# Kernel tuning notes

Hardware: AMD Instinct MI355X
Metric: run time of the kernel (lower is better)

The kernel has to match this reference:

```python
import jax, jax.numpy as jnp
import numpy as np

B, T, H, D = 2, 4096, 16, 64
CHUNK = 64          # chunk_size / prefill_chunk_size
P = 2               # polynomial degree (only deg=2 supported)
SCALE = 0.125       # 1/sqrt(head_dim)
E = D * (D + 1) // 2  # expanded (symmetric) feature dim = 2080

_I, _J = np.triu_indices(D)
_COEF = np.where(_I == _J, 1.0, np.sqrt(2.0)).astype(np.float32)

def _phi(x):
    """Degree-2 symmetric feature map: phi(a).phi(b) == (a.b)**2. [..., D] -> [..., E]."""
    return x[..., _I] * x[..., _J] * jnp.asarray(_COEF, dtype=x.dtype)

def setup_inputs() -> dict:
    rng = jax.random.key(0)
    k0, k1, k2, k3, k4, k5 = jax.random.split(rng, 6)
    query = jax.random.normal(k0, (B, T, H, D), dtype=jnp.float32)
    key = jax.random.normal(k1, (B, T, H, D), dtype=jnp.float32)
    value = jax.random.normal(k2, (B, T, H, D), dtype=jnp.float32)
    # gate holds per-token log decay (log_G): small negative values
    gate = -0.05 * jax.random.uniform(k3, (B, T, H), dtype=jnp.float32)
    initial_state = 0.01 * jax.random.normal(k4, (B, H, E, D), dtype=jnp.float32)
    initial_sk = 0.01 * jax.random.normal(k5, (B, H, E), dtype=jnp.float32)
    return {"query": query, "key": key, "value": value, "gate": gate,
            "initial_state": initial_state, "initial_sk": initial_sk}

def _power_retention(query, key, value, gate, initial_state, initial_sk):
    C = CHUNK
    N = T // C
    # [B,T,H,*] -> chunked [B,H,N,C,*]
    q = query.transpose(0, 2, 1, 3).reshape(B, H, N, C, D)
    k = key.transpose(0, 2, 1, 3).reshape(B, H, N, C, D)
    v = value.transpose(0, 2, 1, 3).reshape(B, H, N, C, D)
    g = gate.transpose(0, 2, 1).reshape(B, H, N, C)

    cg = jnp.cumsum(g, axis=-1)     # cumulative log-gate within chunk [B,H,N,C]
    gsum = cg[..., -1]              # total chunk log-gate [B,H,N]

    # chunk axis to scan position 0
    qs = jnp.moveaxis(q, 2, 0)      # [N,B,H,C,D]
    ks = jnp.moveaxis(k, 2, 0)
    vs = jnp.moveaxis(v, 2, 0)
    cgs = jnp.moveaxis(cg, 2, 0)    # [N,B,H,C]
    gsums = jnp.moveaxis(gsum, 2, 0)  # [N,B,H]

    mask = jnp.tril(jnp.ones((C, C), dtype=bool))

    def step(carry, xs):
        S, sk = carry               # S: [B,H,E,D], sk: [B,H,E]
        qc, kc, vc, cgc, gs = xs    # [B,H,C,D], ..., [B,H,C], [B,H]
        # intra-chunk: degree-2 power attention with gating decay, causal
        qk = jnp.einsum('bhcd,bhmd->bhcm', qc, kc) * SCALE
        dec = jnp.exp(cgc[..., :, None] - cgc[..., None, :])
        s = jnp.where(mask, (qk ** P) * dec, 0.0)
        num = jnp.einsum('bhcm,bhmd->bhcd', s, vc)
        den = s.sum(-1)
        # inter-chunk: read carried state through feature map
        pq = _phi(qc) * (SCALE ** P)           # [B,H,C,E]
        qdec = jnp.exp(cgc)                    # decay from chunk start
        num = num + qdec[..., None] * jnp.einsum('bhce,bhed->bhcd', pq, S)
        den = den + qdec * jnp.einsum('bhce,bhe->bhc', pq, sk)
        # state update: decay old state by full-chunk gate, add new keys
        pk = _phi(kc) * jnp.exp(gs[..., None] - cgc)[..., None]  # [B,H,C,E]
        S = jnp.exp(gs)[..., None, None] * S + jnp.einsum('bhce,bhcd->bhed', pk, vc)
        sk = jnp.exp(gs)[..., None] * sk + pk.sum(2)
        out = num / jnp.maximum(den, 1.0)[..., None]
        return (S, sk), out

    (Sf, skf), outs = jax.lax.scan(jax.checkpoint(step), (initial_state, initial_sk),
                                   (qs, ks, vs, cgs, gsums))
    # outs: [N,B,H,C,D] -> [B,T,H,D]
    out = jnp.moveaxis(outs, 0, 2).reshape(B, H, T, D).transpose(0, 2, 1, 3)
    return out

def reference(query, key, value, gate, initial_state, initial_sk):
    return _power_retention(query, key, value, gate, initial_state, initial_sk)
```

## Files before the change

kernel.cpp:

```cpp
#include <hip/hip_runtime.h>


#define B_ 2
#define T_ 4096
#define H_ 16
#define D_ 64
#define CHUNK_ 64
#define NCH_ 64
#define E_ 2080
#define EH_ 8
#define NBLK_ 36
#define EPAD_ 288
#define NKS_ 9
#define STR_ 296
#define OUTN_ 8388608

typedef __attribute__((ext_vector_type(8))) _Float16 half8v;
typedef __attribute__((ext_vector_type(4))) float floatx4;

union U8 { half8v h; unsigned u[4]; ushort s[8]; };

static __device__ __forceinline__ float wave_iscan(float g, int lane) {
    #pragma unroll
    for (int off = 1; off < 64; off <<= 1) {
        float o = __shfl_up(g, off, 64);
        if (lane >= off) g += o;
    }
    return g;
}

typedef const __attribute__((address_space(1))) unsigned int* gas1_t;
typedef __attribute__((address_space(3))) unsigned int* las3_t;
static __device__ __forceinline__ void gload16(const void* g, void* l) {
    __builtin_amdgcn_global_load_lds((gas1_t)g, (las3_t)l, 16, 0, 0);
}

__global__ __launch_bounds__(256) void prep_kernel(
    const float* __restrict__ q, const float* __restrict__ k, const float* __restrict__ v,
    const float* __restrict__ gate,
    _Float16* __restrict__ qh, _Float16* __restrict__ kh, _Float16* __restrict__ khT,
    _Float16* __restrict__ vhT, float* __restrict__ gse_buf)
{
    const int bid = blockIdx.x;
    const int bh = bid >> 6, n = bid & 63;
    const int b = bh >> 4, h = bh & 15;
    const int t0 = n * CHUNK_;
    const int tid = threadIdx.x;

    __shared__ float cgs[64];
    __shared__ float tbuf[64 * 68];

    if (tid < 64) {
        float g = gate[((size_t)(b * T_ + t0) + tid) * H_ + h];
        cgs[tid] = wave_iscan(g, tid);
    }
    __syncthreads();
    const float gs = cgs[63];
    if (tid == 0) gse_buf[bid] = __expf(gs);

    const int c = tid >> 2, dq = (tid & 3) * 16;
    const size_t gbase = ((size_t)(b * T_ + t0 + c) * H_ + h) * 64 + dq;
    const size_t obase = (size_t)bid * 4096;

    {
        float qsc = 0.125f * __expf(0.5f * cgs[c]);
        #pragma unroll
        for (int g8 = 0; g8 < 2; ++g8) {
            float4 a0 = *(const float4*)(q + gbase + g8 * 8);
            float4 a1 = *(const float4*)(q + gbase + g8 * 8 + 4);
            half8v hv;
            hv[0] = (_Float16)(a0.x * qsc); hv[1] = (_Float16)(a0.y * qsc);
            hv[2] = (_Float16)(a0.z * qsc); hv[3] = (_Float16)(a0.w * qsc);
            hv[4] = (_Float16)(a1.x * qsc); hv[5] = (_Float16)(a1.y * qsc);
            hv[6] = (_Float16)(a1.z * qsc); hv[7] = (_Float16)(a1.w * qsc);
            int grp = (dq >> 3) + g8;
            *(half8v*)&qh[obase + (size_t)(c * 64) + ((grp ^ (c & 7)) << 3)] = hv;
        }
    }
    {
        float ksc = __expf(0.5f * (gs - cgs[c]));
        float4 sa[4];
        #pragma unroll
        for (int i = 0; i < 4; ++i) {
            float4 a = *(const float4*)(k + gbase + i * 4);
            sa[i].x = a.x * ksc; sa[i].y = a.y * ksc;
            sa[i].z = a.z * ksc; sa[i].w = a.w * ksc;
            *(float4*)&tbuf[c * 68 + dq + i * 4] = sa[i];
        }
        #pragma unroll
        for (int g8 = 0; g8 < 2; ++g8) {
            half8v hv;
            hv[0] = (_Float16)sa[g8 * 2].x;     hv[1] = (_Float16)sa[g8 * 2].y;
            hv[2] = (_Float16)sa[g8 * 2].z;     hv[3] = (_Float16)sa[g8 * 2].w;
            hv[4] = (_Float16)sa[g8 * 2 + 1].x; hv[5] = (_Float16)sa[g8 * 2 + 1].y;
            hv[6] = (_Float16)sa[g8 * 2 + 1].z; hv[7] = (_Float16)sa[g8 * 2 + 1].w;
            int grp = (dq >> 3) + g8;
            *(half8v*)&kh[obase + (size_t)(c * 64) + ((grp ^ (c & 7)) << 3)] = hv;
        }
    }
    __syncthreads();
    {
        int d = tid & 63, f = (d & 7) ^ (d >> 3);
        #pragma unroll
        for (int gg = 0; gg < 2; ++gg) {
            int cg = (tid >> 6) * 2 + gg;
            half8v hv;
            #pragma unroll
            for (int j = 0; j < 8; ++j) hv[j] = (_Float16)tbuf[(cg * 8 + j) * 68 + d];
            *(half8v*)&khT[obase + (size_t)(d * 64) + ((cg ^ f) << 3)] = hv;
        }
    }
    __syncthreads();
    {
        #pragma unroll
        for (int i = 0; i < 4; ++i)
            *(float4*)&tbuf[c * 68 + dq + i * 4] = *(const float4*)(v + gbase + i * 4);
    }
    __syncthreads();
    {
        int d = tid & 63, dl = d & 31, f = (dl & 7) ^ (dl >> 3);
        #pragma unroll
        for (int gg = 0; gg < 2; ++gg) {
            int cg = (tid >> 6) * 2 + gg;
            half8v hv;
            #pragma unroll
            for (int j = 0; j < 8; ++j) hv[j] = (_Float16)tbuf[(cg * 8 + j) * 68 + d];
            *(half8v*)&vhT[obase + (size_t)(d * 64) + ((cg ^ f) << 3)] = hv;
        }
    }
}

__global__ __launch_bounds__(512, 2) void scan_kernel(
    const _Float16* __restrict__ qh, const _Float16* __restrict__ khT,
    const _Float16* __restrict__ vhT, const float* __restrict__ gse_buf,
    const float* __restrict__ S0, const float* __restrict__ sk0,
    float* __restrict__ den_buf, _Float16* __restrict__ part)
{
    const int bid = blockIdx.x;
    const int bh = (bid & 7) * 4 + (bid >> 6);
    const int eh = (bid >> 3) & 7;
    const int tid = threadIdx.x, lane = tid & 63, w = tid >> 6;
    const int nlane = lane & 15, quad = lane >> 4;

    __shared__ __align__(16) _Float16 sT[2][64 * STR_];
    __shared__ __align__(16) _Float16 kTs[2][4096];
    __shared__ __align__(16) _Float16 qsh[2][4096];
    __shared__ __align__(16) _Float16 vTs[2][4096];
    __shared__ __align__(16) _Float16 sk_s[2][EPAD_];
    __shared__ int blk_s[NBLK_];

    for (int t = tid; t < NBLK_; t += 512) {
        int g = eh * NBLK_ + t;
        int i = 0;
        while (g >= 8 - (i >> 3)) { g -= 8 - (i >> 3); ++i; }
        int jb = (i >> 3) + g;
        blk_s[t] = i | (jb << 8);
    }
    __syncthreads();

    const _Float16* qsrc = qh + (size_t)(bh * NCH_) * 4096;
    const _Float16* ksrc = khT + (size_t)(bh * NCH_) * 4096;
    const _Float16* vsrc = vhT + (size_t)(bh * NCH_) * 4096;

    gload16(qsrc + tid * 8, &qsh[0][tid * 8]);
    gload16(ksrc + tid * 8, &kTs[0][tid * 8]);
    gload16(vsrc + tid * 8, &vTs[0][tid * 8]);

    for (int e = tid; e < EPAD_; e += 512) {
        int bv = blk_s[e >> 3];
        int i = bv & 255, j8 = (bv >> 8) * 8 + (e & 7);
        float sv = 0.f;
        if (j8 >= i) {
            int er = (i * (129 - i)) / 2 + (j8 - i);
            float coef = (j8 == i) ? 1.f : 1.41421356237f;
            sv = sk0[(size_t)bh * E_ + er] * coef;
        }
        sk_s[0][e] = (_Float16)sv;
    }
    for (int p = tid; p < 64 * EPAD_; p += 512) {
        int d = p / EPAD_;
        int e = p - d * EPAD_;
        int bv = blk_s[e >> 3];
        int i = bv & 255, j8 = (bv >> 8) * 8 + (e & 7);
        float sv = 0.f;
        if (j8 >= i) {
            int er = (i * (129 - i)) / 2 + (j8 - i);
            float coef = (j8 == i) ? 1.f : 1.41421356237f;
            sv = S0[((size_t)bh * E_ + er) * 64 + d] * coef;
        }
        int col8 = e >> 3, gsw = (d >> 2) & 3;
        int pc = ((col8 & ~3) | ((col8 & 3) ^ gsw)) * 8 + (e & 7);
        sT[0][d * STR_ + pc] = (_Float16)sv;
    }

    const int mt = w & 3, nth = w >> 2;
    const int c_row = mt * 16 + nlane;
    const bool den_w = (w < 4);
    const int NTS = (w < 2) ? 3 : 2;

    floatx4 res[3][4];
    floatx4 resk[3];
    #pragma unroll
    for (int ts = 0; ts < 3; ++ts) {
        #pragma unroll
        for (int m = 0; m < 4; ++m) res[ts][m] = (floatx4){0.f, 0.f, 0.f, 0.f};
        resk[ts] = (floatx4){0.f, 0.f, 0.f, 0.f};
        if (ts >= NTS) continue;
        int tile = w + 8 * ts;
        int e = tile * 16 + nlane;
        int bv = blk_s[e >> 3];
        int i = bv & 255, j8 = (bv >> 8) * 8 + (e & 7);
        if (j8 >= i) {
            int er = (i * (129 - i)) / 2 + (j8 - i);
            float coef = (j8 == i) ? 1.f : 1.41421356237f;
            #pragma unroll
            for (int m = 0; m < 4; ++m) {
                floatx4 t4 = *(const floatx4*)&S0[((size_t)bh * E_ + er) * 64 + m * 16 + quad * 4];
                #pragma unroll
                for (int r = 0; r < 4; ++r) res[ts][m][r] = t4[r] * coef;
            }
            if (quad == 0) resk[ts][0] = sk0[(size_t)bh * E_ + er] * coef;
        }
    }

    int qiu_off[NKS_], qrow_off[NKS_];
    #pragma unroll
    for (int ks = 0; ks < NKS_; ++ks) {
        int bv = blk_s[ks * 4 + quad];
        int ib = bv & 255, jb = bv >> 8;
        qiu_off[ks]  = (c_row * 64 + (((ib >> 3) ^ (c_row & 7)) << 3) + (ib & 7)) * 2;
        qrow_off[ks] = (c_row * 64 + ((jb ^ (c_row & 7)) << 3)) * 2;
    }
    const int swzb = (quad ^ ((nlane >> 2) & 3)) << 3;
    const int b0o0 = ((nth * 32 + nlane) * STR_ + swzb) * 2;
    const int b0o1 = ((nth * 32 + 16 + nlane) * STR_ + swzb) * 2;

    int pa_off[3], pb_off[3], stw_off[3], eidx[3];
    unsigned m2sp[3];
    #pragma unroll
    for (int ts = 0; ts < 3; ++ts) {
        pa_off[ts] = pb_off[ts] = stw_off[ts] = eidx[ts] = 0; m2sp[ts] = 0;
        if (ts >= NTS) continue;
        int tile = w + 8 * ts, e = tile * 16 + nlane;
        int bv = blk_s[e >> 3];
        int ib = bv & 255, j8 = (bv >> 8) * 8 + (e & 7);
        int fib = (ib & 7) ^ (ib >> 3), fj8 = (j8 & 7) ^ (j8 >> 3);
        pa_off[ts] = (ib * 64 + ((quad ^ fib) << 3)) * 2;
        pb_off[ts] = (j8 * 64 + ((quad ^ fj8) << 3)) * 2;
        int col8 = e >> 3;
        int pc = ((col8 & ~3) | ((col8 & 3) ^ quad)) * 8 + (e & 7);
        stw_off[ts] = (quad * 4 * STR_ + pc) * 2;
        eidx[ts] = e;
        unsigned hv = (j8 < ib) ? 0u : ((j8 == ib) ? 0x3C00u : 0x4000u);
        m2sp[ts] = (hv << 16) | hv;
    }
    int af_off[4];
    #pragma unroll
    for (int m = 0; m < 4; ++m) {
        int row = m * 16 + nlane, dl = row & 31;
        int fr = (dl & 7) ^ (dl >> 3);
        af_off[m] = (row * 64 + ((quad ^ fr) << 3)) * 2;
    }
    half8v af_sk = (half8v){0, 0, 0, 0, 0, 0, 0, 0};
    if (nlane == 0) af_sk = (half8v){1, 1, 1, 1, 1, 1, 1, 1};

    _Float16* ppart = part + (size_t)eh * OUTN_ + (((size_t)bh * T_) << 6) + nth * 32 + nlane;

    __syncthreads();

    for (int n = 0; n < NCH_; ++n) {
        const int cur = n & 1, nxt = cur ^ 1;

        if (n + 1 < NCH_) {
            gload16(qsrc + (size_t)(n + 1) * 4096 + tid * 8, &qsh[nxt][tid * 8]);
            gload16(ksrc + (size_t)(n + 1) * 4096 + tid * 8, &kTs[nxt][tid * 8]);
            gload16(vsrc + (size_t)(n + 1) * 4096 + tid * 8, &vTs[nxt][tid * 8]);
        }
        const float gsev = gse_buf[bh * NCH_ + n];

        {
            const char* qb = (const char*)&qsh[cur][0];
            const char* sb = (const char*)&sT[cur][0];
            floatx4 acc0 = {0.f, 0.f, 0.f, 0.f};
            floatx4 acc1 = {0.f, 0.f, 0.f, 0.f};
            floatx4 accd = {0.f, 0.f, 0.f, 0.f};
            #pragma unroll
            for (int ks = 0; ks < NKS_; ++ks) {
                ushort qiu = *(const ushort*)(qb + qiu_off[ks]);
                unsigned qi2 = ((unsigned)qiu << 16) | qiu;
                U8 qv; qv.u[0] = qi2; qv.u[1] = qi2; qv.u[2] = qi2; qv.u[3] = qi2;
                half8v qrow = *(const half8v*)(qb + qrow_off[ks]);
                half8v afr = qv.h * qrow;
                half8v b00 = *(const half8v*)(sb + b0o0 + ks * 64);
                half8v b01 = *(const half8v*)(sb + b0o1 + ks * 64);
                acc0 = __builtin_amdgcn_mfma_f32_16x16x32_f16(afr, b00, acc0, 0, 0, 0);
                acc1 = __builtin_amdgcn_mfma_f32_16x16x32_f16(afr, b01, acc1, 0, 0, 0);
                if (den_w) {
                    half8v b1 = (half8v){0, 0, 0, 0, 0, 0, 0, 0};
                    if (nlane == 0) b1 = *(const half8v*)&sk_s[cur][ks * 32 + quad * 8];
                    accd = __builtin_amdgcn_mfma_f32_16x16x32_f16(afr, b1, accd, 0, 0, 0);
                }
            }
            _Float16* pp = ppart + ((size_t)(n * CHUNK_ + mt * 16 + quad * 4) << 6);
            #pragma unroll
            for (int r = 0; r < 4; ++r) {
                pp[(size_t)r << 6] = (_Float16)acc0[r];
                pp[((size_t)r << 6) + 16] = (_Float16)acc1[r];
            }
            if (den_w && nlane == 0) {
                #pragma unroll
                for (int r = 0; r < 4; ++r)
                    atomicAdd(&den_buf[(size_t)bh * T_ + n * CHUNK_ + mt * 16 + quad * 4 + r], accd[r]);
            }
        }

        if (n < NCH_ - 1) {
            const char* kb = (const char*)&kTs[cur][0];
            const char* vb = (const char*)&vTs[cur][0];
            #pragma unroll
            for (int ts = 0; ts < 3; ++ts) {
                if (ts >= NTS) continue;
                #pragma unroll
                for (int m = 0; m < 4; ++m)
                    #pragma unroll
                    for (int r = 0; r < 4; ++r) res[ts][m][r] *= gsev;
                resk[ts][0] *= gsev;
            }
            #pragma unroll
            for (int k2 = 0; k2 < 2; ++k2) {
                const int xo = k2 * 64;
                half8v af0 = *(const half8v*)(vb + (af_off[0] ^ xo));
                half8v af1 = *(const half8v*)(vb + (af_off[1] ^ xo));
                half8v af2 = *(const half8v*)(vb + (af_off[2] ^ xo));
                half8v af3 = *(const half8v*)(vb + (af_off[3] ^ xo));
                #pragma unroll
                for (int ts = 0; ts < 3; ++ts) {
                    if (ts >= NTS) continue;
                    half8v pa = *(const half8v*)(kb + (pa_off[ts] ^ xo));
                    half8v pb = *(const half8v*)(kb + (pb_off[ts] ^ xo));
                    U8 mv; mv.u[0] = m2sp[ts]; mv.u[1] = m2sp[ts]; mv.u[2] = m2sp[ts]; mv.u[3] = m2sp[ts];
                    half8v bfr = pa * pb * mv.h;
                    res[ts][0] = __builtin_amdgcn_mfma_f32_16x16x32_f16(af0, bfr, res[ts][0], 0, 0, 0);
                    res[ts][1] = __builtin_amdgcn_mfma_f32_16x16x32_f16(af1, bfr, res[ts][1], 0, 0, 0);
                    res[ts][2] = __builtin_amdgcn_mfma_f32_16x16x32_f16(af2, bfr, res[ts][2], 0, 0, 0);
                    res[ts][3] = __builtin_amdgcn_mfma_f32_16x16x32_f16(af3, bfr, res[ts][3], 0, 0, 0);
                    resk[ts] = __builtin_amdgcn_mfma_f32_16x16x32_f16(af_sk, bfr, resk[ts], 0, 0, 0);
                }
            }
            char* stb = (char*)&sT[nxt][0];
            #pragma unroll
            for (int ts = 0; ts < 3; ++ts) {
                if (ts >= NTS) continue;
                #pragma unroll
                for (int m = 0; m < 4; ++m)
                    #pragma unroll
                    for (int r = 0; r < 4; ++r)
                        *(_Float16*)(stb + stw_off[ts] + (m * 16 * STR_ + r * STR_) * 2) =
                            (_Float16)res[ts][m][r];
                if (quad == 0) sk_s[nxt][eidx[ts]] = (_Float16)resk[ts][0];
            }
        }

        __syncthreads();
    }
}

__global__ __launch_bounds__(256) void intra_merge_kernel(
    const _Float16* __restrict__ qh, const _Float16* __restrict__ kh,
    const _Float16* __restrict__ vhT, const float* __restrict__ gse_buf,
    const float* __restrict__ den_buf, const _Float16* __restrict__ part,
    float* __restrict__ out)
{
    const int bid = blockIdx.x;
    const int n = bid & 63, h = (bid >> 6) & 15, b = bid >> 10;
    const int tid = threadIdx.x;
    const int lane = tid & 63, w = tid >> 6;
    const int nlane = lane & 15, quad = lane >> 4;
    const int t0 = n * CHUNK_;
    const int bh = b * H_ + h;

    __shared__ __align__(16) _Float16 qs[4096];
    __shared__ __align__(16) _Float16 ksm[4096];
    __shared__ __align__(16) _Float16 vs[4096];
    __shared__ __align__(16) _Float16 ss[4096];
    __shared__ float nbuf[64 * 68];
    __shared__ float dens[64];

    const size_t obase = (size_t)(bh * NCH_ + n) * 4096;
    gload16(qh + obase + tid * 8, &qs[tid * 8]);
    gload16(qh + obase + 2048 + tid * 8, &qs[2048 + tid * 8]);
    gload16(kh + obase + tid * 8, &ksm[tid * 8]);
    gload16(kh + obase + 2048 + tid * 8, &ksm[2048 + tid * 8]);
    gload16(vhT + obase + tid * 8, &vs[tid * 8]);
    gload16(vhT + obase + 2048 + tid * 8, &vs[2048 + tid * 8]);
    const float gsei = 1.0f / gse_buf[bh * NCH_ + n];
    __syncthreads();

    const int ct = w;
    const int crow = ct * 16 + nlane;
    const int cswz = crow & 7;

    floatx4 qk[4];
    #pragma unroll
    for (int mt = 0; mt < 4; ++mt) qk[mt] = (floatx4){0.f, 0.f, 0.f, 0.f};
    #pragma unroll
    for (int ks_ = 0; ks_ < 2; ++ks_) {
        int g = ks_ * 4 + quad;
        half8v a = *(const half8v*)&qs[crow * 64 + ((g ^ cswz) << 3)];
        #pragma unroll
        for (int mt = 0; mt < 4; ++mt) {
            int mrow = mt * 16 + nlane;
            half8v bf = *(const half8v*)&ksm[mrow * 64 + ((g ^ (mrow & 7)) << 3)];
            qk[mt] = __builtin_amdgcn_mfma_f32_16x16x32_f16(a, bf, qk[mt], 0, 0, 0);
        }
    }

    float dsum[4] = {0.f, 0.f, 0.f, 0.f};
    #pragma unroll
    for (int mt = 0; mt < 4; ++mt) {
        int m = mt * 16 + nlane;
        #pragma unroll
        for (int r = 0; r < 4; ++r) {
            int c = ct * 16 + quad * 4 + r;
            float sv = qk[mt][r];
            sv = sv * sv * gsei;
            sv = (m <= c) ? sv : 0.f;
            dsum[r] += sv;
            ss[c * 64 + (((m >> 3) ^ (c & 7)) << 3) + (m & 7)] = (_Float16)sv;
        }
    }
    #pragma unroll
    for (int off = 1; off < 16; off <<= 1)
        #pragma unroll
        for (int r = 0; r < 4; ++r) dsum[r] += __shfl_xor(dsum[r], off, 64);
    if (nlane == 0) {
        #pragma unroll
        for (int r = 0; r < 4; ++r) dens[ct * 16 + quad * 4 + r] = dsum[r];
    }
    __syncthreads();

    floatx4 num[4];
    #pragma unroll
    for (int dt = 0; dt < 4; ++dt) num[dt] = (floatx4){0.f, 0.f, 0.f, 0.f};
    #pragma unroll
    for (int ks_ = 0; ks_ < 2; ++ks_) {
        int g = ks_ * 4 + quad;
        half8v a = *(const half8v*)&ss[crow * 64 + ((g ^ cswz) << 3)];
        #pragma unroll
        for (int dt = 0; dt < 4; ++dt) {
            int d = dt * 16 + nlane, dl = d & 31;
            int f = (dl & 7) ^ (dl >> 3);
            half8v bf = *(const half8v*)&vs[d * 64 + ((g ^ f) << 3)];
            num[dt] = __builtin_amdgcn_mfma_f32_16x16x32_f16(a, bf, num[dt], 0, 0, 0);
        }
    }
    #pragma unroll
    for (int dt = 0; dt < 4; ++dt)
        #pragma unroll
        for (int r = 0; r < 4; ++r)
            nbuf[(ct * 16 + quad * 4 + r) * 68 + dt * 16 + nlane] = num[dt][r];
    __syncthreads();

    for (int idx = tid; idx < 512; idx += 256) {
        int c = idx >> 3, g = idx & 7;
        float acc8[8];
        #pragma unroll
        for (int j = 0; j < 8; ++j) acc8[j] = nbuf[c * 68 + g * 8 + j];
        size_t pb = (((size_t)bh * T_ + t0 + c) << 6) + g * 8;
        #pragma unroll
        for (int ehh = 0; ehh < EH_; ++ehh) {
            half8v pv = *(const half8v*)&part[(size_t)ehh * OUTN_ + pb];
            #pragma unroll
            for (int j = 0; j < 8; ++j) acc8[j] += (float)pv[j];
        }
        float den = dens[c] + den_buf[(size_t)bh * T_ + t0 + c];
        float rden = 1.0f / fmaxf(den, 1.0f);
        float4 o0, o1;
        o0.x = acc8[0] * rden; o0.y = acc8[1] * rden;
        o0.z = acc8[2] * rden; o0.w = acc8[3] * rden;
        o1.x = acc8[4] * rden; o1.y = acc8[5] * rden;
        o1.z = acc8[6] * rden; o1.w = acc8[7] * rden;
        float* op = &out[((size_t)(b * T_ + t0 + c) * H_ + h) * 64 + g * 8];
        *(float4*)op = o0;
        *((float4*)op + 1) = o1;
    }
}

extern "C" void kernel_launch(void* const* d_in, const int* in_sizes, int n_in,
                              void* d_out, int out_size, void* d_ws, size_t ws_size,
                              hipStream_t stream)
{
    (void)in_sizes; (void)n_in; (void)out_size; (void)ws_size;
    const float* q   = (const float*)d_in[0];
    const float* k   = (const float*)d_in[1];
    const float* v   = (const float*)d_in[2];
    const float* g   = (const float*)d_in[3];
    const float* S0  = (const float*)d_in[4];
    const float* sk0 = (const float*)d_in[5];
    float* out = (float*)d_out;

    char* wp = (char*)d_ws;
    float*    den_buf = (float*)wp;                 wp += (size_t)B_ * H_ * T_ * sizeof(float);
    _Float16* part    = (_Float16*)wp;              wp += (size_t)EH_ * OUTN_ * sizeof(_Float16);
    _Float16* qh      = (_Float16*)wp;              wp += (size_t)B_ * H_ * T_ * D_ * sizeof(_Float16);
    _Float16* khT     = (_Float16*)wp;              wp += (size_t)B_ * H_ * T_ * D_ * sizeof(_Float16);
    _Float16* vhT     = (_Float16*)wp;              wp += (size_t)B_ * H_ * T_ * D_ * sizeof(_Float16);
    _Float16* kh      = (_Float16*)wp;              wp += (size_t)B_ * H_ * T_ * D_ * sizeof(_Float16);
    float*    gse_buf = (float*)wp;

    hipMemsetAsync(den_buf, 0, (size_t)B_ * H_ * T_ * sizeof(float), stream);
    prep_kernel<<<dim3(2048), dim3(256), 0, stream>>>(q, k, v, g, qh, kh, khT, vhT, gse_buf);
    scan_kernel<<<dim3(256), dim3(512), 0, stream>>>(qh, khT, vhT, gse_buf, S0, sk0, den_buf, part);
    intra_merge_kernel<<<dim3(2048), dim3(256), 0, stream>>>(qh, kh, vhT, gse_buf, den_buf, part, out);
}
```

Baseline: 399.6 us.

## Warp-specialize intra_merge so extra waves load partials while MFMA waves compute

The merge kernel grows to 512 threads. Waves 0-3 do the intra-chunk QK^T and SV MFMA work, while waves 4-7 load and reduce the eight fp16 partial-output slices from global memory into a second shared buffer at the same time. The aim is to hide the global read latency of the partials behind the intra-chunk matmuls. The cost is more shared memory (an extra 17KB buffer) and a larger block, which may lower occupancy.

```diff
diff --git a/kernel.cpp b/kernel.cpp
--- a/kernel.cpp
+++ b/kernel.cpp
@@ -365,7 +365,7 @@
     }
 }
 
-__global__ __launch_bounds__(256) void intra_merge_kernel(
+__global__ __launch_bounds__(512) void intra_merge_kernel(
     const _Float16* __restrict__ qh, const _Float16* __restrict__ kh,
     const _Float16* __restrict__ vhT, const float* __restrict__ gse_buf,
     const float* __restrict__ den_buf, const _Float16* __restrict__ part,
@@ -384,102 +384,121 @@
     __shared__ __align__(16) _Float16 vs[4096];
     __shared__ __align__(16) _Float16 ss[4096];
     __shared__ float nbuf[64 * 68];
+    __shared__ float nbuf2[64 * 68];
     __shared__ float dens[64];
 
     const size_t obase = (size_t)(bh * NCH_ + n) * 4096;
     gload16(qh + obase + tid * 8, &qs[tid * 8]);
-    gload16(qh + obase + 2048 + tid * 8, &qs[2048 + tid * 8]);
     gload16(kh + obase + tid * 8, &ksm[tid * 8]);
-    gload16(kh + obase + 2048 + tid * 8, &ksm[2048 + tid * 8]);
     gload16(vhT + obase + tid * 8, &vs[tid * 8]);
-    gload16(vhT + obase + 2048 + tid * 8, &vs[2048 + tid * 8]);
     const float gsei = 1.0f / gse_buf[bh * NCH_ + n];
     __syncthreads();
 
-    const int ct = w;
-    const int crow = ct * 16 + nlane;
-    const int cswz = crow & 7;
-
-    floatx4 qk[4];
-    #pragma unroll
-    for (int mt = 0; mt < 4; ++mt) qk[mt] = (floatx4){0.f, 0.f, 0.f, 0.f};
-    #pragma unroll
-    for (int ks_ = 0; ks_ < 2; ++ks_) {
-        int g = ks_ * 4 + quad;
-        half8v a = *(const half8v*)&qs[crow * 64 + ((g ^ cswz) << 3)];
+    if (w < 4) {
+        const int ct = w;
+        const int crow = ct * 16 + nlane;
+        const int cswz = crow & 7;
+        floatx4 qk[4];
+        #pragma unroll
+        for (int mt = 0; mt < 4; ++mt) qk[mt] = (floatx4){0.f, 0.f, 0.f, 0.f};
+        #pragma unroll
+        for (int ks_ = 0; ks_ < 2; ++ks_) {
+            int g = ks_ * 4 + quad;
+            half8v a = *(const half8v*)&qs[crow * 64 + ((g ^ cswz) << 3)];
+            #pragma unroll
+            for (int mt = 0; mt < 4; ++mt) {
+                int mrow = mt * 16 + nlane;
+                half8v bf = *(const half8v*)&ksm[mrow * 64 + ((g ^ (mrow & 7)) << 3)];
+                qk[mt] = __builtin_amdgcn_mfma_f32_16x16x32_f16(a, bf, qk[mt], 0, 0, 0);
+            }
+        }
+        float dsum[4] = {0.f, 0.f, 0.f, 0.f};
         #pragma unroll
         for (int mt = 0; mt < 4; ++mt) {
-            int mrow = mt * 16 + nlane;
-            half8v bf = *(const half8v*)&ksm[mrow * 64 + ((g ^ (mrow & 7)) << 3)];
-            qk[mt] = __builtin_amdgcn_mfma_f32_16x16x32_f16(a, bf, qk[mt], 0, 0, 0);
-        }
-    }
-
-    float dsum[4] = {0.f, 0.f, 0.f, 0.f};
-    #pragma unroll
-    for (int mt = 0; mt < 4; ++mt) {
-        int m = mt * 16 + nlane;
-        #pragma unroll
-        for (int r = 0; r < 4; ++r) {
-            int c = ct * 16 + quad * 4 + r;
-            float sv = qk[mt][r];
-            sv = sv * sv * gsei;
-            sv = (m <= c) ? sv : 0.f;
-            dsum[r] += sv;
-            ss[c * 64 + (((m >> 3) ^ (c & 7)) << 3) + (m & 7)] = (_Float16)sv;
-        }
-    }
-    #pragma unroll
-    for (int off = 1; off < 16; off <<= 1)
-        #pragma unroll
-        for (int r = 0; r < 4; ++r) dsum[r] += __shfl_xor(dsum[r], off, 64);
-    if (nlane == 0) {
-        #pragma unroll
-        for (int r = 0; r < 4; ++r) dens[ct * 16 + quad * 4 + r] = dsum[r];
-    }
-    __syncthreads();
-
-    floatx4 num[4];
-    #pragma unroll
-    for (int dt = 0; dt < 4; ++dt) num[dt] = (floatx4){0.f, 0.f, 0.f, 0.f};
-    #pragma unroll
-    for (int ks_ = 0; ks_ < 2; ++ks_) {
-        int g = ks_ * 4 + quad;
-        half8v a = *(const half8v*)&ss[crow * 64 + ((g ^ cswz) << 3)];
-        #pragma unroll
-        for (int dt = 0; dt < 4; ++dt) {
-            int d = dt * 16 + nlane, dl = d & 31;
-            int f = (dl & 7) ^ (dl >> 3);
-            half8v bf = *(const half8v*)&vs[d * 64 + ((g ^ f) << 3)];
-            num[dt] = __builtin_amdgcn_mfma_f32_16x16x32_f16(a, bf, num[dt], 0, 0, 0);
-        }
-    }
-    #pragma unroll
-    for (int dt = 0; dt < 4; ++dt)
-        #pragma unroll
-        for (int r = 0; r < 4; ++r)
-            nbuf[(ct * 16 + quad * 4 + r) * 68 + dt * 16 + nlane] = num[dt][r];
-    __syncthreads();
-
-    for (int idx = tid; idx < 512; idx += 256) {
-        int c = idx >> 3, g = idx & 7;
-        float acc8[8];
-        #pragma unroll
-        for (int j = 0; j < 8; ++j) acc8[j] = nbuf[c * 68 + g * 8 + j];
-        size_t pb = (((size_t)bh * T_ + t0 + c) << 6) + g * 8;
-        #pragma unroll
-        for (int ehh = 0; ehh < EH_; ++ehh) {
-            half8v pv = *(const half8v*)&part[(size_t)ehh * OUTN_ + pb];
-            #pragma unroll
-            for (int j = 0; j < 8; ++j) acc8[j] += (float)pv[j];
-        }
+            int m = mt * 16 + nlane;
+            #pragma unroll
+            for (int r = 0; r < 4; ++r) {
+                int c = ct * 16 + quad * 4 + r;
+                float sv = qk[mt][r];
+                sv = sv * sv * gsei;
+                sv = (m <= c) ? sv : 0.f;
+                dsum[r] += sv;
+                ss[c * 64 + (((m >> 3) ^ (c & 7)) << 3) + (m & 7)] = (_Float16)sv;
+            }
+        }
+        #pragma unroll
+        for (int off = 1; off < 16; off <<= 1)
+            #pragma unroll
+            for (int r = 0; r < 4; ++r) dsum[r] += __shfl_xor(dsum[r], off, 64);
+        if (nlane == 0) {
+            #pragma unroll
+            for (int r = 0; r < 4; ++r) dens[ct * 16 + quad * 4 + r] = dsum[r];
+        }
+    } else {
+        const int t2 = tid - 256;
+        #pragma unroll
+        for (int it = 0; it < 2; ++it) {
+            int idx = t2 + it * 256;
+            int c = idx >> 3, g = idx & 7;
+            float acc8[8];
+            #pragma unroll
+            for (int j = 0; j < 8; ++j) acc8[j] = 0.f;
+            size_t pb = (((size_t)bh * T_ + t0 + c) << 6) + g * 8;
+            #pragma unroll
+            for (int ehh = 0; ehh < EH_; ++ehh) {
+                half8v pv = *(const half8v*)&part[(size_t)ehh * OUTN_ + pb];
+                #pragma unroll
+                for (int j = 0; j < 8; ++j) acc8[j] += (float)pv[j];
+            }
+            float4 s0, s1;
+            s0.x = acc8[0]; s0.y = acc8[1]; s0.z = acc8[2]; s0.w = acc8[3];
+            s1.x = acc8[4]; s1.y = acc8[5]; s1.z = acc8[6]; s1.w = acc8[7];
+            *(float4*)&nbuf2[c * 68 + g * 8] = s0;
+            *(float4*)&nbuf2[c * 68 + g * 8 + 4] = s1;
+        }
+    }
+    __syncthreads();
+
+    if (w < 4) {
+        const int ct = w;
+        const int crow = ct * 16 + nlane;
+        const int cswz = crow & 7;
+        floatx4 num[4];
+        #pragma unroll
+        for (int dt = 0; dt < 4; ++dt) num[dt] = (floatx4){0.f, 0.f, 0.f, 0.f};
+        #pragma unroll
+        for (int ks_ = 0; ks_ < 2; ++ks_) {
+            int g = ks_ * 4 + quad;
+            half8v a = *(const half8v*)&ss[crow * 64 + ((g ^ cswz) << 3)];
+            #pragma unroll
+            for (int dt = 0; dt < 4; ++dt) {
+                int d = dt * 16 + nlane, dl = d & 31;
+                int f = (dl & 7) ^ (dl >> 3);
+                half8v bf = *(const half8v*)&vs[d * 64 + ((g ^ f) << 3)];
+                num[dt] = __builtin_amdgcn_mfma_f32_16x16x32_f16(a, bf, num[dt], 0, 0, 0);
+            }
+        }
+        #pragma unroll
+        for (int dt = 0; dt < 4; ++dt)
+            #pragma unroll
+            for (int r = 0; r < 4; ++r)
+                nbuf[(ct * 16 + quad * 4 + r) * 68 + dt * 16 + nlane] = num[dt][r];
+    }
+    __syncthreads();
+
+    {
+        int c = tid >> 3, g = tid & 7;
+        float4 a0 = *(const float4*)&nbuf[c * 68 + g * 8];
+        float4 a1 = *(const float4*)&nbuf[c * 68 + g * 8 + 4];
+        float4 b0 = *(const float4*)&nbuf2[c * 68 + g * 8];
+        float4 b1 = *(const float4*)&nbuf2[c * 68 + g * 8 + 4];
         float den = dens[c] + den_buf[(size_t)bh * T_ + t0 + c];
         float rden = 1.0f / fmaxf(den, 1.0f);
         float4 o0, o1;
-        o0.x = acc8[0] * rden; o0.y = acc8[1] * rden;
-        o0.z = acc8[2] * rden; o0.w = acc8[3] * rden;
-        o1.x = acc8[4] * rden; o1.y = acc8[5] * rden;
-        o1.z = acc8[6] * rden; o1.w = acc8[7] * rden;
+        o0.x = (a0.x + b0.x) * rden; o0.y = (a0.y + b0.y) * rden;
+        o0.z = (a0.z + b0.z) * rden; o0.w = (a0.w + b0.w) * rden;
+        o1.x = (a1.x + b1.x) * rden; o1.y = (a1.y + b1.y) * rden;
+        o1.z = (a1.z + b1.z) * rden; o1.w = (a1.w + b1.w) * rden;
         float* op = &out[((size_t)(b * T_ + t0 + c) * H_ + h) * 64 + g * 8];
         *(float4*)op = o0;
         *((float4*)op + 1) = o1;
@@ -511,5 +530,5 @@
     hipMemsetAsync(den_buf, 0, (size_t)B_ * H_ * T_ * sizeof(float), stream);
     prep_kernel<<<dim3(2048), dim3(256), 0, stream>>>(q, k, v, g, qh, kh, khT, vhT, gse_buf);
     scan_kernel<<<dim3(256), dim3(512), 0, stream>>>(qh, khT, vhT, gse_buf, S0, sk0, den_buf, part);
-    intra_merge_kernel<<<dim3(2048), dim3(256), 0, stream>>>(qh, kh, vhT, gse_buf, den_buf, part, out);
+    intra_merge_kernel<<<dim3(2048), dim3(512), 0, stream>>>(qh, kh, vhT, gse_buf, den_buf, part, out);
 }
```

New measurement: 402.5 us. Within noise of the previous version (+0.7%).
